# Optimization experiments

Measured on AMD Instinct MI355X. Metric: run time of the kernel, lower is better.

## Reference

```python
import jax, jax.numpy as jnp
import numpy as np

N = 500000  # nodes (groups of k edges)
K = 32      # edges per node == MLP input width
E = N * K
H = 256     # hidden size


def setup_inputs() -> dict:
    key = jax.random.key(0)
    ks = jax.random.split(key, 12)
    def lin(kw, fan_in, fan_out):
        # torch nn.Linear default init: U(-1/sqrt(fan_in), 1/sqrt(fan_in))
        bound = 1.0 / np.sqrt(fan_in)
        return jax.random.uniform(kw, (fan_in, fan_out), jnp.float32, -bound, bound)
    return {
        "x": jax.random.normal(ks[0], (N, 3), jnp.float32),
        "edge_index": jax.random.randint(ks[1], (2, E), 0, N, jnp.int32),
        "edge_attr": jax.random.normal(ks[2], (E, 1), jnp.float32),
        "W1": lin(ks[3], K, H), "b1": jnp.zeros((H,), jnp.float32),
        "W2": lin(ks[4], H, H), "b2": jnp.zeros((H,), jnp.float32),
        "W3": lin(ks[5], H, H), "b3": jnp.zeros((H,), jnp.float32),
        "W4": lin(ks[6], H, 1), "b4": jnp.zeros((1,), jnp.float32),
    }


def reference(x, edge_index, edge_attr, W1, b1, W2, b2, W3, b3, W4, b4):
    # message() returns edge_attr; aggregate() reshapes all messages to (-1, k)
    # (index is ignored), then runs the 4-layer MLP. x/edge_index unused in math.
    g = edge_attr.reshape(-1, K)                      # [N, K]
    h = jnp.tanh(g @ W1 + b1)                         # [N, H]
    h = jnp.tanh(h @ W2 + b2)                         # [N, H]
    h = jnp.tanh(h @ W3 + b3)                         # [N, H]
    out = jax.nn.log_sigmoid(h @ W4 + b4)             # [N, 1]
    return jnp.squeeze(out, 1)                        # [N]
```

## Files before the change

### kernel.cpp

```cpp
#include <hip/hip_runtime.h>
#include <stdint.h>

#define NN 500000
#define HH 256
#define MBLK 64
#define NBLK ((NN + MBLK - 1) / MBLK)
#define CHUNK_U32 8192
#define NCHUNK 17

typedef short short8 __attribute__((ext_vector_type(8)));
typedef float floatx4 __attribute__((ext_vector_type(4)));

__device__ __forceinline__ unsigned short f2bf(float f) {
  union { float f; uint32_t u; } v; v.f = f;
  uint32_t r = v.u + 0x7fffu + ((v.u >> 16) & 1u);
  return (unsigned short)(r >> 16);
}
__device__ __forceinline__ float bf2f(unsigned short h) {
  union { uint32_t u; float f; } v; v.u = ((uint32_t)h) << 16;
  return v.f;
}
__device__ __forceinline__ float tanh_fast(float x) {
  float xc = fminf(fmaxf(x, -9.0f), 9.0f);
  float e = __expf(2.0f * xc);
  return __fdividef(e - 1.0f, e + 1.0f);
}
__device__ __forceinline__ float log_sigmoid_f(float x) {
  return fminf(x, 0.0f) - log1pf(__expf(-fabsf(x)));
}

__global__ void __launch_bounds__(256)
pack_weights(const float* __restrict__ W1, const float* __restrict__ W2,
             const float* __restrict__ W3, uint16_t* __restrict__ ws16) {
  int t = blockIdx.x * 256 + threadIdx.x;
  if (t >= NCHUNK * CHUNK_U32) return;
  int chunk = t >> 13;
  int r = t & 8191;
  int n  = r & 255;
  int kp = r >> 8;
  float w;
  if (chunk == 0)      w = W1[kp * HH + n];
  else if (chunk <= 8) w = W2[((chunk - 1) * 32 + kp) * HH + n];
  else                 w = W3[((chunk - 9) * 32 + kp) * HH + n];
  unsigned short hi = f2bf(w);
  unsigned short lo = f2bf(w - bf2f(hi));
  uint16_t* row = ws16 + (size_t)chunk * 16384 + n * 64;
  row[((((kp >> 3)    ) ^ (n & 7)) << 3) | (kp & 7)] = hi;
  row[(((4 + (kp >> 3)) ^ (n & 7)) << 3) | (kp & 7)] = lo;
}

__device__ __forceinline__ void stage_chunk(const uint32_t* __restrict__ src,
                                            uint32_t* dst, int wave, int lane) {
#pragma unroll
  for (int it = 0; it < 4; ++it) {
    int o = (wave * 4 + it) * 256;
    __builtin_amdgcn_global_load_lds(
        (const __attribute__((address_space(1))) uint32_t*)(src + o + lane * 4),
        (__attribute__((address_space(3))) uint32_t*)(dst + o), 16, 0, 0);
  }
}

#define KSTEP(AHI, ALO, WB)                                                    \
  {                                                                            \
    const char* wb8 = (const char*)(WB);                                       \
    _Pragma("unroll")                                                          \
    for (int nt = 0; nt < 4; ++nt) {                                           \
      int nr = cb + nt * 16 + c;                                               \
      short8 bhi = *(const short8*)(wb8 + nr * 128 + ((q ^ (nr & 7)) << 4));   \
      short8 blo = *(const short8*)(wb8 + nr * 128 + (((4 + q) ^ (nr & 7)) << 4)); \
      _Pragma("unroll")                                                        \
      for (int mt = 0; mt < 2; ++mt) {                                         \
        acc[mt][nt] = __builtin_amdgcn_mfma_f32_16x16x32_bf16(AHI[mt], bhi, acc[mt][nt], 0, 0, 0); \
        acc[mt][nt] = __builtin_amdgcn_mfma_f32_16x16x32_bf16(ALO[mt], bhi, acc[mt][nt], 0, 0, 0); \
        acc[mt][nt] = __builtin_amdgcn_mfma_f32_16x16x32_bf16(AHI[mt], blo, acc[mt][nt], 0, 0, 0); \
      }                                                                        \
    }                                                                          \
  }

#define ZEROACC()                                                              \
  {                                                                            \
    _Pragma("unroll") for (int mt = 0; mt < 2; ++mt)                           \
        _Pragma("unroll") for (int nt = 0; nt < 4; ++nt)                       \
            acc[mt][nt] = (floatx4){0.f, 0.f, 0.f, 0.f};                       \
  }

#define EPILOGUE_PACK(BIAS)                                                    \
  {                                                                            \
    _Pragma("unroll")                                                          \
    for (int nt = 0; nt < 4; ++nt) {                                           \
      float bv = (BIAS)[cb + nt * 16 + c];                                     \
      _Pragma("unroll")                                                        \
      for (int mt = 0; mt < 2; ++mt) {                                         \
        _Pragma("unroll")                                                      \
        for (int rr = 0; rr < 4; ++rr) {                                       \
          float tv = tanh_fast(acc[mt][nt][rr] + bv);                          \
          unsigned short h_ = f2bf(tv);                                        \
          unsigned short l_ = f2bf(tv - bf2f(h_));                             \
          int row = wr * 32 + mt * 16 + q * 4 + rr;                            \
          int k = cb + nt * 16 + c;                                            \
          hbuf[row * 256 + ((((k >> 2) ^ (row & 15)) << 2) | (k & 3))] =       \
              (uint32_t)h_ | ((uint32_t)l_ << 16);                             \
        }                                                                      \
      }                                                                        \
    }                                                                          \
  }

__global__ void __launch_bounds__(512, 2)
mlp_fused(const float* __restrict__ ea, const float* __restrict__ b1,
          const float* __restrict__ b2, const float* __restrict__ b3,
          const float* __restrict__ W4, const float* __restrict__ b4p,
          const uint32_t* __restrict__ wsw, float* __restrict__ out) {
  __shared__ uint32_t smem[32768];
  uint32_t* hbuf = smem;
  uint32_t* wbuf = smem + 16384;

  const int tid = threadIdx.x;
  const int wave = tid >> 6;
  const int lane = tid & 63;
  const int q = lane >> 4;
  const int c = lane & 15;
  const int wr = wave >> 2;
  const int wc = wave & 3;
  const int cb = wc * 64;
  const int blk = blockIdx.x;

  floatx4 acc[2][4];

  stage_chunk(wsw, wbuf, wave, lane);
  short8 g_hi[2], g_lo[2];
#pragma unroll
  for (int mt = 0; mt < 2; ++mt) {
    int row = blk * 64 + wr * 32 + mt * 16 + c;
    if (row >= NN) row = NN - 1;
    const float* gp = ea + (size_t)row * 32 + q * 8;
    floatx4 v0 = *(const floatx4*)gp;
    floatx4 v1 = *(const floatx4*)(gp + 4);
    float g8[8] = {v0[0], v0[1], v0[2], v0[3], v1[0], v1[1], v1[2], v1[3]};
#pragma unroll
    for (int j = 0; j < 8; ++j) {
      unsigned short h_ = f2bf(g8[j]);
      g_hi[mt][j] = (short)h_;
      g_lo[mt][j] = (short)f2bf(g8[j] - bf2f(h_));
    }
  }
  __syncthreads();

  stage_chunk(wsw + CHUNK_U32, wbuf + CHUNK_U32, wave, lane);
  ZEROACC();
  KSTEP(g_hi, g_lo, wbuf);
  EPILOGUE_PACK(b1);
  __syncthreads();

#pragma unroll 1
  for (int lay = 0; lay < 2; ++lay) {
    const int ch0 = 1 + lay * 8;
    ZEROACC();
#pragma unroll 1
    for (int kc = 0; kc < 8; ++kc) {
      const int chunk = ch0 + kc;
      const uint32_t* wcur = wbuf + (chunk & 1) * CHUNK_U32;
      if (chunk + 1 < NCHUNK)
        stage_chunk(wsw + (chunk + 1) * CHUNK_U32,
                    wbuf + ((chunk + 1) & 1) * CHUNK_U32, wave, lane);
      short8 ahi[2], alo[2];
#pragma unroll
      for (int mt = 0; mt < 2; ++mt) {
        const int row = wr * 32 + mt * 16 + c;
        const uint32_t* hb = hbuf + row * 256;
        const int g0 = kc * 8 + q * 2;
        uint4 p0 = *(const uint4*)(hb + (((g0) ^ (row & 15)) << 2));
        uint4 p1 = *(const uint4*)(hb + (((g0 + 1) ^ (row & 15)) << 2));
        uint32_t u[8] = {p0.x, p0.y, p0.z, p0.w, p1.x, p1.y, p1.z, p1.w};
#pragma unroll
        for (int j = 0; j < 8; ++j) {
          ahi[mt][j] = (short)(u[j] & 0xffffu);
          alo[mt][j] = (short)(u[j] >> 16);
        }
      }
      KSTEP(ahi, alo, wcur);
      __syncthreads();
    }
    if (lay == 0) {
      EPILOGUE_PACK(b2);
      __syncthreads();
    }
  }

  float p[2][4];
#pragma unroll
  for (int mt = 0; mt < 2; ++mt)
#pragma unroll
    for (int rr = 0; rr < 4; ++rr) p[mt][rr] = 0.0f;
#pragma unroll
  for (int nt = 0; nt < 4; ++nt) {
    float bv = b3[cb + nt * 16 + c];
    float wv = W4[cb + nt * 16 + c];
#pragma unroll
    for (int mt = 0; mt < 2; ++mt)
#pragma unroll
      for (int rr = 0; rr < 4; ++rr)
        p[mt][rr] += tanh_fast(acc[mt][nt][rr] + bv) * wv;
  }
#pragma unroll
  for (int off = 1; off < 16; off <<= 1)
#pragma unroll
    for (int mt = 0; mt < 2; ++mt)
#pragma unroll
      for (int rr = 0; rr < 4; ++rr)
        p[mt][rr] += __shfl_xor(p[mt][rr], off, 64);
  float* red = (float*)hbuf;
  if (c == 0) {
#pragma unroll
    for (int mt = 0; mt < 2; ++mt)
#pragma unroll
      for (int rr = 0; rr < 4; ++rr)
        red[wc * 64 + wr * 32 + mt * 16 + q * 4 + rr] = p[mt][rr];
  }
  __syncthreads();
  if (tid < 64) {
    int row = blk * 64 + tid;
    float s = red[tid] + red[64 + tid] + red[128 + tid] + red[192 + tid] + b4p[0];
    if (row < NN) out[row] = log_sigmoid_f(s);
  }
}

extern "C" void kernel_launch(void* const* d_in, const int* in_sizes, int n_in,
                              void* d_out, int out_size, void* d_ws, size_t ws_size,
                              hipStream_t stream) {
  const float* ea = (const float*)d_in[2];
  const float* W1 = (const float*)d_in[3];
  const float* b1 = (const float*)d_in[4];
  const float* W2 = (const float*)d_in[5];
  const float* b2 = (const float*)d_in[6];
  const float* W3 = (const float*)d_in[7];
  const float* b3 = (const float*)d_in[8];
  const float* W4 = (const float*)d_in[9];
  const float* b4 = (const float*)d_in[10];

  pack_weights<<<(NCHUNK * CHUNK_U32 + 255) / 256, 256, 0, stream>>>(
      W1, W2, W3, (uint16_t*)d_ws);
  mlp_fused<<<NBLK, 512, 0, stream>>>(ea, b1, b2, b3, W4, b4,
                                      (const uint32_t*)d_ws, (float*)d_out);
}
```

Before: 907.9 us.

## Read weight fragments directly from global memory instead of staging through LDS

Weight chunks are no longer double-buffered into shared memory with global_load_lds. Each lane now loads its bf16 hi/lo B fragments directly from a repacked global layout, which is expected to hit in L2. This halves LDS use to the activation buffer only, drops the per-chunk barriers, fully unrolls the k-chunk loop, and raises the launch bound to 4 blocks per CU. The trade-off is more global/L2 load latency and traffic per MFMA step and higher register pressure, in return for more occupancy and less synchronisation.

```diff
diff --git a/kernel.cpp b/kernel.cpp
--- a/kernel.cpp
+++ b/kernel.cpp
@@ -3,10 +3,8 @@
 
 #define NN 500000
 #define HH 256
-#define MBLK 64
-#define NBLK ((NN + MBLK - 1) / MBLK)
-#define CHUNK_U32 8192
-#define NCHUNK 17
+#define NBLK ((NN + 63) / 64)
+#define NCH 17
 
 typedef short short8 __attribute__((ext_vector_type(8)));
 typedef float floatx4 __attribute__((ext_vector_type(4)));
@@ -33,41 +31,29 @@
 pack_weights(const float* __restrict__ W1, const float* __restrict__ W2,
              const float* __restrict__ W3, uint16_t* __restrict__ ws16) {
   int t = blockIdx.x * 256 + threadIdx.x;
-  if (t >= NCHUNK * CHUNK_U32) return;
-  int chunk = t >> 13;
+  if (t >= NCH * 8192) return;
+  int ch = t >> 13;
   int r = t & 8191;
   int n  = r & 255;
   int kp = r >> 8;
   float w;
-  if (chunk == 0)      w = W1[kp * HH + n];
-  else if (chunk <= 8) w = W2[((chunk - 1) * 32 + kp) * HH + n];
-  else                 w = W3[((chunk - 9) * 32 + kp) * HH + n];
+  if (ch == 0)      w = W1[kp * HH + n];
+  else if (ch <= 8) w = W2[((ch - 1) * 32 + kp) * HH + n];
+  else              w = W3[((ch - 9) * 32 + kp) * HH + n];
   unsigned short hi = f2bf(w);
   unsigned short lo = f2bf(w - bf2f(hi));
-  uint16_t* row = ws16 + (size_t)chunk * 16384 + n * 64;
-  row[((((kp >> 3)    ) ^ (n & 7)) << 3) | (kp & 7)] = hi;
-  row[(((4 + (kp >> 3)) ^ (n & 7)) << 3) | (kp & 7)] = lo;
-}
-
-__device__ __forceinline__ void stage_chunk(const uint32_t* __restrict__ src,
-                                            uint32_t* dst, int wave, int lane) {
-#pragma unroll
-  for (int it = 0; it < 4; ++it) {
-    int o = (wave * 4 + it) * 256;
-    __builtin_amdgcn_global_load_lds(
-        (const __attribute__((address_space(1))) uint32_t*)(src + o + lane * 4),
-        (__attribute__((address_space(3))) uint32_t*)(dst + o), 16, 0, 0);
-  }
-}
-
-#define KSTEP(AHI, ALO, WB)                                                    \
+  uint16_t* p = ws16 + (size_t)ch * 16384 + n * 32 + kp;
+  p[0]    = hi;
+  p[8192] = lo;
+}
+
+#define KSTEP_G(AHI, ALO, WG)                                                  \
   {                                                                            \
-    const char* wb8 = (const char*)(WB);                                       \
+    const uint16_t* wg_ = (WG);                                                \
     _Pragma("unroll")                                                          \
     for (int nt = 0; nt < 4; ++nt) {                                           \
-      int nr = cb + nt * 16 + c;                                               \
-      short8 bhi = *(const short8*)(wb8 + nr * 128 + ((q ^ (nr & 7)) << 4));   \
-      short8 blo = *(const short8*)(wb8 + nr * 128 + (((4 + q) ^ (nr & 7)) << 4)); \
+      short8 bhi = *(const short8*)(wg_ + woff + nt * 512);                    \
+      short8 blo = *(const short8*)(wg_ + 8192 + woff + nt * 512);             \
       _Pragma("unroll")                                                        \
       for (int mt = 0; mt < 2; ++mt) {                                         \
         acc[mt][nt] = __builtin_amdgcn_mfma_f32_16x16x32_bf16(AHI[mt], bhi, acc[mt][nt], 0, 0, 0); \
@@ -105,14 +91,12 @@
     }                                                                          \
   }
 
-__global__ void __launch_bounds__(512, 2)
+__global__ void __launch_bounds__(512, 4)
 mlp_fused(const float* __restrict__ ea, const float* __restrict__ b1,
           const float* __restrict__ b2, const float* __restrict__ b3,
           const float* __restrict__ W4, const float* __restrict__ b4p,
-          const uint32_t* __restrict__ wsw, float* __restrict__ out) {
-  __shared__ uint32_t smem[32768];
-  uint32_t* hbuf = smem;
-  uint32_t* wbuf = smem + 16384;
+          const uint16_t* __restrict__ wsw, float* __restrict__ out) {
+  __shared__ uint32_t hbuf[16384];
 
   const int tid = threadIdx.x;
   const int wave = tid >> 6;
@@ -123,10 +107,10 @@
   const int wc = wave & 3;
   const int cb = wc * 64;
   const int blk = blockIdx.x;
+  const int woff = (cb + c) * 32 + q * 8;
 
   floatx4 acc[2][4];
 
-  stage_chunk(wsw, wbuf, wave, lane);
   short8 g_hi[2], g_lo[2];
 #pragma unroll
   for (int mt = 0; mt < 2; ++mt) {
@@ -143,25 +127,18 @@
       g_lo[mt][j] = (short)f2bf(g8[j] - bf2f(h_));
     }
   }
-  __syncthreads();
-
-  stage_chunk(wsw + CHUNK_U32, wbuf + CHUNK_U32, wave, lane);
+
   ZEROACC();
-  KSTEP(g_hi, g_lo, wbuf);
+  KSTEP_G(g_hi, g_lo, wsw);
   EPILOGUE_PACK(b1);
   __syncthreads();
 
 #pragma unroll 1
   for (int lay = 0; lay < 2; ++lay) {
-    const int ch0 = 1 + lay * 8;
     ZEROACC();
-#pragma unroll 1
+#pragma unroll
     for (int kc = 0; kc < 8; ++kc) {
-      const int chunk = ch0 + kc;
-      const uint32_t* wcur = wbuf + (chunk & 1) * CHUNK_U32;
-      if (chunk + 1 < NCHUNK)
-        stage_chunk(wsw + (chunk + 1) * CHUNK_U32,
-                    wbuf + ((chunk + 1) & 1) * CHUNK_U32, wave, lane);
+      const uint16_t* wg = wsw + (size_t)(1 + lay * 8 + kc) * 16384;
       short8 ahi[2], alo[2];
 #pragma unroll
       for (int mt = 0; mt < 2; ++mt) {
@@ -177,10 +154,10 @@
           alo[mt][j] = (short)(u[j] >> 16);
         }
       }
-      KSTEP(ahi, alo, wcur);
-      __syncthreads();
+      KSTEP_G(ahi, alo, wg);
     }
     if (lay == 0) {
+      __syncthreads();
       EPILOGUE_PACK(b2);
       __syncthreads();
     }
@@ -208,6 +185,7 @@
 #pragma unroll
       for (int rr = 0; rr < 4; ++rr)
         p[mt][rr] += __shfl_xor(p[mt][rr], off, 64);
+  __syncthreads();
   float* red = (float*)hbuf;
   if (c == 0) {
 #pragma unroll
@@ -237,8 +215,8 @@
   const float* W4 = (const float*)d_in[9];
   const float* b4 = (const float*)d_in[10];
 
-  pack_weights<<<(NCHUNK * CHUNK_U32 + 255) / 256, 256, 0, stream>>>(
+  pack_weights<<<(NCH * 8192 + 255) / 256, 256, 0, stream>>>(
       W1, W2, W3, (uint16_t*)d_ws);
   mlp_fused<<<NBLK, 512, 0, stream>>>(ea, b1, b2, b3, W4, b4,
-                                      (const uint32_t*)d_ws, (float*)d_out);
-}
+                                      (const uint16_t*)d_ws, (float*)d_out);
+}
```

Result: faster. 764.1 us (-15.8%).
